# Performance work log

Hardware: AMD Instinct MI355X
Metric: run time of the kernel (lower is better)

Reference implementation:

```python
import jax, jax.numpy as jnp
import numpy as np

KDIM = 8192
EPS = 1e-8  # F.cosine_similarity default eps


def _encoder(x, W1, b1, W2, b2, W3, b3):
    # x: [..., KDIM] -> [..., 128]; Linear(KDIM,512)->ReLU->Linear(512,256)->ReLU->Linear(256,128)
    h = jax.nn.relu(x @ W1 + b1)
    h = jax.nn.relu(h @ W2 + b2)
    return h @ W3 + b3


def setup_inputs() -> dict:
    key = jax.random.key(0)
    ks = jax.random.split(key, 16)

    def lin(k, fan_in, fan_out):
        bound = 1.0 / np.sqrt(fan_in)
        kw, kb = jax.random.split(k)
        W = jax.random.uniform(kw, (fan_in, fan_out), jnp.float32, -bound, bound)
        b = jax.random.uniform(kb, (fan_out,), jnp.float32, -bound, bound)
        return W, b

    W1, b1 = lin(ks[0], KDIM, 512)
    W2, b2 = lin(ks[1], 512, 256)
    W3, b3 = lin(ks[2], 256, 128)
    Wi1, bi1 = lin(ks[3], 128 + 6, 64)
    Wi2, bi2 = lin(ks[4], 64, 32)
    Wi3, bi3 = lin(ks[5], 32, 1)

    return {
        "new_knowledge": jax.random.normal(ks[6], (KDIM,), jnp.float32),
        "existing_knowledge": jax.random.normal(ks[7], (10, KDIM), jnp.float32),
        "math_metrics": jax.random.uniform(ks[8], (6,), jnp.float32),
        "W1": W1, "b1": b1, "W2": W2, "b2": b2, "W3": W3, "b3": b3,
        "Wi1": Wi1, "bi1": bi1, "Wi2": Wi2, "bi2": bi2, "Wi3": Wi3, "bi3": bi3,
    }


def reference(new_knowledge, existing_knowledge, math_metrics,
              W1, b1, W2, b2, W3, b3, Wi1, bi1, Wi2, bi2, Wi3, bi3):
    # Encode new knowledge: [128]
    new_enc = _encoder(new_knowledge, W1, b1, W2, b2, W3, b3)
    # Batched encode of the (up to 10) existing knowledge vectors: [10, 128]
    ex_enc = _encoder(existing_knowledge, W1, b1, W2, b2, W3, b3)

    # Per-item geometric distance (L2 norm of difference)
    diff = new_enc[None, :] - ex_enc                     # [10, 128]
    geo_dist = jnp.sqrt(jnp.sum(diff * diff, axis=-1))   # [10]

    # Per-item cosine similarity with torch eps clamping
    new_n = jnp.maximum(jnp.linalg.norm(new_enc), EPS)
    ex_n = jnp.maximum(jnp.linalg.norm(ex_enc, axis=-1), EPS)  # [10]
    cos = (ex_enc @ new_enc) / (new_n * ex_n)            # [10]

    avg_consistency = jnp.mean(geo_dist - cos)

    # Mathematical-constraint integrator MLP on [128 + 6]
    combined = jnp.concatenate([new_enc, math_metrics])  # [134]
    h = jax.nn.relu(combined @ Wi1 + bi1)
    h = jax.nn.relu(h @ Wi2 + bi2)
    quality = h @ Wi3 + bi3                              # [1]

    integration_loss = jnp.exp(-quality)                 # [1]
    total = jnp.squeeze(avg_consistency + integration_loss)
    return total
```

## Files before the change

kernel.cpp:

```cpp
#include <hip/hip_runtime.h>
#include <math.h>

#define EPS 1e-8f
#define MAGIC 0x1F2E3D4C
typedef float f32x4 __attribute__((ext_vector_type(4)));

__device__ __forceinline__ float wredsum(float v) {
#pragma unroll
  for (int o = 32; o > 0; o >>= 1) v += __shfl_down(v, o, 64);
  return v;
}

__device__ __forceinline__ void waitflag(const int* f) {
  while (__hip_atomic_load(f, __ATOMIC_RELAXED, __HIP_MEMORY_SCOPE_AGENT) !=
         MAGIC)
    __builtin_amdgcn_s_sleep(2);
}

__device__ __forceinline__ void fma8(const float4* w, const float4 a,
                                     const float4 b, float4& c) {
  const float xs[8] = {a.x, a.y, a.z, a.w, b.x, b.y, b.z, b.w};
#pragma unroll
  for (int i = 0; i < 8; ++i) {
    c.x = fmaf(xs[i], w[i].x, c.x);
    c.y = fmaf(xs[i], w[i].y, c.y);
    c.z = fmaf(xs[i], w[i].z, c.z);
    c.w = fmaf(xs[i], w[i].w, c.w);
  }
}

__global__ __launch_bounds__(256, 2) void k_l1(const float* __restrict__ xn,
                                               const float* __restrict__ xe,
                                               const float* __restrict__ W1,
                                               float* __restrict__ p1,
                                               int* __restrict__ flg) {
  if (blockIdx.x == 0 && blockIdx.y == 0 && threadIdx.x < 40)
    flg[threadIdx.x] = 0;
  __shared__ float red[11 * 32 * 36];
  const int cg  = threadIdx.x & 7;
  const int ks  = threadIdx.x >> 3;
  const int col = blockIdx.x * 32 + cg * 4;
  const int k0  = blockIdx.y * 256 + ks * 8;

  float4 w[8];
#pragma unroll
  for (int i = 0; i < 8; ++i)
    w[i] = *(const float4*)&W1[(size_t)(k0 + i) * 512 + col];

  float4 acc[11];
#pragma unroll
  for (int r = 0; r < 11; ++r) acc[r] = make_float4(0.f, 0.f, 0.f, 0.f);
  {
    const float4 a = *(const float4*)&xn[k0];
    const float4 b = *(const float4*)&xn[k0 + 4];
    fma8(w, a, b, acc[0]);
  }
#pragma unroll
  for (int r = 0; r < 10; ++r) {
    const float4 a = *(const float4*)&xe[r * 8192 + k0];
    const float4 b = *(const float4*)&xe[r * 8192 + k0 + 4];
    fma8(w, a, b, acc[r + 1]);
  }

#pragma unroll
  for (int r = 0; r < 11; ++r)
    *(float4*)&red[(r * 32 + ks) * 36 + cg * 4] = acc[r];
  __syncthreads();

  for (int o = threadIdx.x; o < 352; o += 256) {
    const int r = o >> 5, c = o & 31;
    float s = 0.f;
#pragma unroll
    for (int k = 0; k < 32; ++k) s += red[(r * 32 + k) * 36 + c];
    p1[((size_t)blockIdx.y * 11 + r) * 512 + blockIdx.x * 32 + c] = s;
  }
}

__global__ __launch_bounds__(256) void k_tail(
    const float* __restrict__ p1, const float* __restrict__ b1,
    const float* __restrict__ W2, const float* __restrict__ b2,
    const float* __restrict__ W3, const float* __restrict__ b3,
    const float* __restrict__ mm,
    const float* __restrict__ Wi1, const float* __restrict__ bi1,
    const float* __restrict__ Wi2, const float* __restrict__ bi2,
    const float* __restrict__ Wi3, const float* __restrict__ bi3,
    float* __restrict__ p2, float* __restrict__ encp,
    int* __restrict__ flg, float* __restrict__ out) {
  __shared__ __align__(16) float smem[12672];
  const int t = threadIdx.x;
  const int j = blockIdx.x;

  if (j < 32) {
    float w2r[16];
#pragma unroll
    for (int i = 0; i < 16; ++i)
      w2r[i] = W2[(size_t)(j * 16 + i) * 256 + t];

    float* h1s = smem;
    if (t < 176) {
      const int r = t >> 4, cc = t & 15;
      const int col = j * 16 + cc;
      float s = b1[col];
#pragma unroll
      for (int ch = 0; ch < 32; ++ch)
        s += p1[(size_t)(ch * 11 + r) * 512 + col];
      h1s[r * 16 + cc] = fmaxf(s, 0.f);
    }
    __syncthreads();

    float acc[11];
#pragma unroll
    for (int r = 0; r < 11; ++r) acc[r] = 0.f;
#pragma unroll
    for (int kk = 0; kk < 16; ++kk) {
#pragma unroll
      for (int r = 0; r < 11; ++r)
        acc[r] = fmaf(h1s[r * 16 + kk], w2r[kk], acc[r]);
    }
    const int q = t >> 5, cc = t & 31;
#pragma unroll
    for (int r = 0; r < 11; ++r)
      p2[((size_t)q * 32 + j) * 352 + r * 32 + cc] = acc[r];

    __syncthreads();
    if (t == 0) {
      __threadfence();
      __hip_atomic_store(&flg[j], MAGIC, __ATOMIC_RELAXED,
                         __HIP_MEMORY_SCOPE_AGENT);
    }
    return;
  }

  if (j < 40) {
    const int q = j - 32;
    const int c3 = t & 127, half = t >> 7;
    float w3r[16];
#pragma unroll
    for (int i = 0; i < 16; ++i)
      w3r[i] = W3[(size_t)(q * 32 + half * 16 + i) * 128 + c3];

    if (t < 32) waitflag(&flg[t]);
    __syncthreads();
    if (t == 0) __threadfence();
    __syncthreads();

    float* h2q = smem;
    for (int o = t; o < 352; o += 256) {
      const int r = o >> 5, kk = o & 31;
      float s = b2[q * 32 + kk];
#pragma unroll
      for (int jj = 0; jj < 32; ++jj)
        s += p2[((size_t)q * 32 + jj) * 352 + r * 32 + kk];
      h2q[r * 32 + kk] = fmaxf(s, 0.f);
    }
    __syncthreads();

    float* redB = smem + 512;
    {
      float acc[11];
#pragma unroll
      for (int r = 0; r < 11; ++r) acc[r] = 0.f;
#pragma unroll
      for (int i = 0; i < 16; ++i) {
        const int kk = half * 16 + i;
#pragma unroll
        for (int r = 0; r < 11; ++r)
          acc[r] = fmaf(h2q[r * 32 + kk], w3r[i], acc[r]);
      }
#pragma unroll
      for (int r = 0; r < 11; ++r) redB[(half * 11 + r) * 128 + c3] = acc[r];
    }
    __syncthreads();
    for (int o = t; o < 1408; o += 256)
      encp[(size_t)q * 1408 + o] = redB[o] + redB[1408 + o];

    __syncthreads();
    if (t == 0) {
      __threadfence();
      __hip_atomic_store(&flg[32 + q], MAGIC, __ATOMIC_RELAXED,
                         __HIP_MEMORY_SCOPE_AGENT);
    }
    return;
  }

  float* encs = smem;
  float* wi1s = smem + 1536;
  float* wi2s = smem + 10112;
  float* comb = smem + 12160;
  float* h1b  = smem + 12296;
  for (int i = t; i < 2144; i += 256)
    ((f32x4*)wi1s)[i] = ((const f32x4*)Wi1)[i];
  for (int i = t; i < 512; i += 256)
    ((f32x4*)wi2s)[i] = ((const f32x4*)Wi2)[i];

  if (t < 8) waitflag(&flg[32 + t]);
  __syncthreads();
  if (t == 0) __threadfence();
  __syncthreads();

  for (int o = t; o < 1408; o += 256) {
    float s = b3[o & 127];
#pragma unroll
    for (int g = 0; g < 8; ++g) s += encp[(size_t)g * 1408 + o];
    encs[o] = s;
  }
  __syncthreads();

  float consist = 0.f;
  float n0 = 0.f, n1 = 0.f;
  if (t < 64) {
    n0 = encs[t]; n1 = encs[64 + t];
    comb[t] = n0; comb[64 + t] = n1;
    if (t < 6) comb[128 + t] = mm[t];
  }
  __syncthreads();
  if (t < 64) {
    const float nn = wredsum(n0 * n0 + n1 * n1);
#pragma unroll
    for (int r = 1; r <= 10; ++r) {
      const float e0 = encs[r * 128 + t];
      const float e1 = encs[r * 128 + 64 + t];
      const float d0 = e0 - n0, d1 = e1 - n1;
      const float g  = wredsum(d0 * d0 + d1 * d1);
      const float qq = wredsum(e0 * e0 + e1 * e1);
      const float dd = wredsum(e0 * n0 + e1 * n1);
      if (t == 0) {
        const float geo = sqrtf(g);
        const float den = fmaxf(sqrtf(nn), EPS) * fmaxf(sqrtf(qq), EPS);
        consist += geo - dd / den;
      }
    }
  } else if (t < 128) {
    const int tt = t - 64;
    float hh = bi1[tt];
#pragma unroll 4
    for (int k = 0; k < 134; ++k) hh = fmaf(comb[k], wi1s[k * 64 + tt], hh);
    h1b[tt] = fmaxf(hh, 0.f);
  }
  __syncthreads();
  if (t < 64) {
    float part = 0.f;
    if (t < 32) {
      float hh = bi2[t];
#pragma unroll 8
      for (int k = 0; k < 64; ++k) hh = fmaf(h1b[k], wi2s[k * 32 + t], hh);
      part = fmaxf(hh, 0.f) * Wi3[t];
    }
    const float qual = wredsum(part);
    if (t == 0) out[0] = consist * 0.1f + expf(-(qual + bi3[0]));
  }
}

extern "C" void kernel_launch(void* const* d_in, const int* in_sizes, int n_in,
                              void* d_out, int out_size, void* d_ws, size_t ws_size,
                              hipStream_t stream) {
  (void)in_sizes; (void)n_in; (void)out_size; (void)ws_size;
  const float* xn  = (const float*)d_in[0];
  const float* xe  = (const float*)d_in[1];
  const float* mm  = (const float*)d_in[2];
  const float* W1  = (const float*)d_in[3];
  const float* b1  = (const float*)d_in[4];
  const float* W2  = (const float*)d_in[5];
  const float* b2  = (const float*)d_in[6];
  const float* W3  = (const float*)d_in[7];
  const float* b3  = (const float*)d_in[8];
  const float* Wi1 = (const float*)d_in[9];
  const float* bi1 = (const float*)d_in[10];
  const float* Wi2 = (const float*)d_in[11];
  const float* bi2 = (const float*)d_in[12];
  const float* Wi3 = (const float*)d_in[13];
  const float* bi3 = (const float*)d_in[14];
  float* out = (float*)d_out;

  char* ws = (char*)d_ws;
  float* p1   = (float*)(ws);
  float* p2   = (float*)(ws + 720896);
  float* encp = (float*)(ws + 1081344);
  int*   flg  = (int*)  (ws + 1126400);

  hipLaunchKernelGGL(k_l1,   dim3(16, 32), dim3(256), 0, stream,
                     xn, xe, W1, p1, flg);
  hipLaunchKernelGGL(k_tail, dim3(41),     dim3(256), 0, stream,
                     p1, b1, W2, b2, W3, b3, mm,
                     Wi1, bi1, Wi2, bi2, Wi3, bi3, p2, encp, flg, out);
}
```

Measured before the change: 110.7 us.

## Replace layer-3 split blocks with atomic H2 accumulation and single-block tail

Layer-2 blocks now atomically add their partial products into one shared H2 accumulator and bump a completion counter, instead of writing per-block partials that are later reduced. The eight separate layer-3 blocks and their flag handshakes are removed, and the final block computes the full 256x128 layer-3 product itself after waiting for the counter. Layer-2 blocks also issue a dummy W3 load so W3 is warmed in cache for the tail. A memset is added to zero the accumulator, and the tail now performs serial layer-3 work in one block. Float atomics make the summation order nondeterministic.

```diff
diff --git a/kernel.cpp b/kernel.cpp
--- a/kernel.cpp
+++ b/kernel.cpp
@@ -2,19 +2,12 @@
 #include <math.h>
 
 #define EPS 1e-8f
-#define MAGIC 0x1F2E3D4C
 typedef float f32x4 __attribute__((ext_vector_type(4)));
 
 __device__ __forceinline__ float wredsum(float v) {
 #pragma unroll
   for (int o = 32; o > 0; o >>= 1) v += __shfl_down(v, o, 64);
   return v;
-}
-
-__device__ __forceinline__ void waitflag(const int* f) {
-  while (__hip_atomic_load(f, __ATOMIC_RELAXED, __HIP_MEMORY_SCOPE_AGENT) !=
-         MAGIC)
-    __builtin_amdgcn_s_sleep(2);
 }
 
 __device__ __forceinline__ void fma8(const float4* w, const float4 a,
@@ -32,10 +25,7 @@
 __global__ __launch_bounds__(256, 2) void k_l1(const float* __restrict__ xn,
                                                const float* __restrict__ xe,
                                                const float* __restrict__ W1,
-                                               float* __restrict__ p1,
-                                               int* __restrict__ flg) {
-  if (blockIdx.x == 0 && blockIdx.y == 0 && threadIdx.x < 40)
-    flg[threadIdx.x] = 0;
+                                               float* __restrict__ p1) {
   __shared__ float red[11 * 32 * 36];
   const int cg  = threadIdx.x & 7;
   const int ks  = threadIdx.x >> 3;
@@ -84,13 +74,16 @@
     const float* __restrict__ Wi1, const float* __restrict__ bi1,
     const float* __restrict__ Wi2, const float* __restrict__ bi2,
     const float* __restrict__ Wi3, const float* __restrict__ bi3,
-    float* __restrict__ p2, float* __restrict__ encp,
-    int* __restrict__ flg, float* __restrict__ out) {
-  __shared__ __align__(16) float smem[12672];
+    float* __restrict__ H2acc, int* __restrict__ cnt,
+    float* __restrict__ out) {
+  __shared__ __align__(16) float smem[15104];
   const int t = threadIdx.x;
   const int j = blockIdx.x;
 
   if (j < 32) {
+    float dead = ((const f32x4*)W3)[j * 256 + t][0];
+    asm volatile("" ::"v"(dead));
+
     float w2r[16];
 #pragma unroll
     for (int i = 0; i < 16; ++i)
@@ -117,92 +110,54 @@
       for (int r = 0; r < 11; ++r)
         acc[r] = fmaf(h1s[r * 16 + kk], w2r[kk], acc[r]);
     }
-    const int q = t >> 5, cc = t & 31;
-#pragma unroll
-    for (int r = 0; r < 11; ++r)
-      p2[((size_t)q * 32 + j) * 352 + r * 32 + cc] = acc[r];
+#pragma unroll
+    for (int r = 0; r < 11; ++r) atomicAdd(&H2acc[r * 256 + t], acc[r]);
 
     __syncthreads();
     if (t == 0) {
       __threadfence();
-      __hip_atomic_store(&flg[j], MAGIC, __ATOMIC_RELAXED,
-                         __HIP_MEMORY_SCOPE_AGENT);
+      __hip_atomic_fetch_add(cnt, 1, __ATOMIC_ACQ_REL,
+                             __HIP_MEMORY_SCOPE_AGENT);
     }
     return;
   }
 
-  if (j < 40) {
-    const int q = j - 32;
-    const int c3 = t & 127, half = t >> 7;
-    float w3r[16];
-#pragma unroll
-    for (int i = 0; i < 16; ++i)
-      w3r[i] = W3[(size_t)(q * 32 + half * 16 + i) * 128 + c3];
-
-    if (t < 32) waitflag(&flg[t]);
-    __syncthreads();
-    if (t == 0) __threadfence();
-    __syncthreads();
-
-    float* h2q = smem;
-    for (int o = t; o < 352; o += 256) {
-      const int r = o >> 5, kk = o & 31;
-      float s = b2[q * 32 + kk];
-#pragma unroll
-      for (int jj = 0; jj < 32; ++jj)
-        s += p2[((size_t)q * 32 + jj) * 352 + r * 32 + kk];
-      h2q[r * 32 + kk] = fmaxf(s, 0.f);
-    }
-    __syncthreads();
-
-    float* redB = smem + 512;
-    {
-      float acc[11];
-#pragma unroll
-      for (int r = 0; r < 11; ++r) acc[r] = 0.f;
-#pragma unroll
-      for (int i = 0; i < 16; ++i) {
-        const int kk = half * 16 + i;
-#pragma unroll
-        for (int r = 0; r < 11; ++r)
-          acc[r] = fmaf(h2q[r * 32 + kk], w3r[i], acc[r]);
-      }
-#pragma unroll
-      for (int r = 0; r < 11; ++r) redB[(half * 11 + r) * 128 + c3] = acc[r];
-    }
-    __syncthreads();
-    for (int o = t; o < 1408; o += 256)
-      encp[(size_t)q * 1408 + o] = redB[o] + redB[1408 + o];
-
-    __syncthreads();
-    if (t == 0) {
-      __threadfence();
-      __hip_atomic_store(&flg[32 + q], MAGIC, __ATOMIC_RELAXED,
-                         __HIP_MEMORY_SCOPE_AGENT);
-    }
-    return;
-  }
-
-  float* encs = smem;
-  float* wi1s = smem + 1536;
-  float* wi2s = smem + 10112;
-  float* comb = smem + 12160;
-  float* h1b  = smem + 12296;
+  float* wi1s = smem;
+  float* wi2s = smem + 8576;
+  float* h2s  = smem + 10624;
+  float* encs = smem + 13440;
+  float* comb = smem + 14848;
+  float* h1b  = smem + 14982;
   for (int i = t; i < 2144; i += 256)
     ((f32x4*)wi1s)[i] = ((const f32x4*)Wi1)[i];
   for (int i = t; i < 512; i += 256)
     ((f32x4*)wi2s)[i] = ((const f32x4*)Wi2)[i];
 
-  if (t < 8) waitflag(&flg[32 + t]);
-  __syncthreads();
-  if (t == 0) __threadfence();
-  __syncthreads();
-
-  for (int o = t; o < 1408; o += 256) {
-    float s = b3[o & 127];
-#pragma unroll
-    for (int g = 0; g < 8; ++g) s += encp[(size_t)g * 1408 + o];
-    encs[o] = s;
+  if (t == 0) {
+    while (__hip_atomic_load(cnt, __ATOMIC_RELAXED,
+                             __HIP_MEMORY_SCOPE_AGENT) < 32)
+      __builtin_amdgcn_s_sleep(2);
+    __threadfence();
+  }
+  __syncthreads();
+
+  for (int o = t; o < 2816; o += 256)
+    h2s[o] = fmaxf(H2acc[o] + b2[o & 255], 0.f);
+  __syncthreads();
+
+  if (t < 128) {
+    float eacc[11];
+#pragma unroll
+    for (int r = 0; r < 11; ++r) eacc[r] = 0.f;
+    for (int k = 0; k < 256; ++k) {
+      const float w = W3[(size_t)k * 128 + t];
+#pragma unroll
+      for (int r = 0; r < 11; ++r)
+        eacc[r] = fmaf(h2s[r * 256 + k], w, eacc[r]);
+    }
+    const float bb = b3[t];
+#pragma unroll
+    for (int r = 0; r < 11; ++r) encs[r * 128 + t] = eacc[r] + bb;
   }
   __syncthreads();
 
@@ -273,14 +228,14 @@
   float* out = (float*)d_out;
 
   char* ws = (char*)d_ws;
-  float* p1   = (float*)(ws);
-  float* p2   = (float*)(ws + 720896);
-  float* encp = (float*)(ws + 1081344);
-  int*   flg  = (int*)  (ws + 1126400);
-
+  float* p1    = (float*)(ws);
+  float* H2acc = (float*)(ws + 720896);
+  int*   cnt   = (int*)  (ws + 732160);
+
+  hipMemsetAsync(ws + 720896, 0, 11268, stream);
   hipLaunchKernelGGL(k_l1,   dim3(16, 32), dim3(256), 0, stream,
-                     xn, xe, W1, p1, flg);
-  hipLaunchKernelGGL(k_tail, dim3(41),     dim3(256), 0, stream,
+                     xn, xe, W1, p1);
+  hipLaunchKernelGGL(k_tail, dim3(33),     dim3(256), 0, stream,
                      p1, b1, W2, b2, W3, b3, mm,
-                     Wi1, bi1, Wi2, bi2, Wi3, bi3, p2, encp, flg, out);
-}
+                     Wi1, bi1, Wi2, bi2, Wi3, bi3, H2acc, cnt, out);
+}
```

Result: slower. 127.6 us (+15.3%).
